# Performance work log

Measured on AMD Instinct MI355X. Metric: run time of the kernel, lower is better.

Reference implementation:

```python
import jax, jax.numpy as jnp
import numpy as np

B, N, D, H, M = 4, 4096, 1024, 16, 128
DH = D // H  # 64
SCALE = DH ** -0.5


def setup_inputs() -> dict:
    key = jax.random.key(0)
    ks = jax.random.split(key, 8)
    std = 0.02
    x = jax.random.normal(ks[0], (B, N, D), dtype=jnp.float32)
    W_qkv = jax.random.normal(ks[1], (D, 3 * D), dtype=jnp.float32) * std
    W_gate = jax.random.normal(ks[2], (D, H), dtype=jnp.float32) * std
    b_gate = jnp.zeros((H,), dtype=jnp.float32)
    agent_tokens = jax.random.normal(ks[3], (H, M, DH), dtype=jnp.float32) * std
    W_qa = jax.random.normal(ks[4], (H, H), dtype=jnp.float32) * std  # 1x1 conv over heads
    W_ak = jax.random.normal(ks[5], (H, H), dtype=jnp.float32) * std
    W_out = jax.random.normal(ks[6], (D, D), dtype=jnp.float32) * std
    mask = jnp.ones((B, N), dtype=bool)
    return {"x": x, "W_qkv": W_qkv, "W_gate": W_gate, "b_gate": b_gate,
            "agent_tokens": agent_tokens, "W_qa": W_qa, "W_ak": W_ak,
            "W_out": W_out, "mask": mask}


def reference(x, W_qkv, W_gate, b_gate, agent_tokens, W_qa, W_ak, W_out, mask):
    # qkv projection: b n (qkv h d) -> qkv b h n d
    qkv = (x @ W_qkv).reshape(B, N, 3, H, DH)
    qkv = jnp.transpose(qkv, (2, 0, 3, 1, 4))  # (3, B, H, N, DH)
    q, k, v = qkv[0], qkv[1], qkv[2]

    a = agent_tokens * SCALE  # (H, M, DH), broadcast over batch

    qa_sim = jnp.einsum('bhid,hjd->bhij', q, a)  # (B, H, N, M)
    ak_sim = jnp.einsum('hid,bhjd->bhij', a, k)  # (B, H, M, N)

    max_neg = -jnp.finfo(ak_sim.dtype).max
    ak_sim = jnp.where(mask[:, None, None, :], ak_sim, max_neg)

    qa_attn = jax.nn.softmax(qa_sim, axis=-1)
    ak_attn = jax.nn.softmax(ak_sim, axis=-1)

    # talking heads: 1x1 conv over head channel
    qa_attn = jnp.einsum('gh,bhij->bgij', W_qa, qa_attn)
    ak_attn = jnp.einsum('gh,bhij->bgij', W_ak, ak_attn)

    agent_gathered = jnp.einsum('bhij,bhjd->bhid', ak_attn, v)      # (B, H, M, DH)
    out = jnp.einsum('bhij,bhjd->bhid', qa_attn, agent_gathered)     # (B, H, N, DH)

    out = jnp.where(mask[:, None, :, None], out, 0.0)

    gates = jax.nn.sigmoid(x @ W_gate + b_gate)          # (B, N, H)
    out = out * jnp.transpose(gates, (0, 2, 1))[..., None]  # (B, H, N, 1)

    out = jnp.transpose(out, (0, 2, 1, 3)).reshape(B, N, D) @ W_out
    return out, agent_gathered
```

## Files before the change

kernel.cpp:

```cpp
#include <hip/hip_runtime.h>

#define B_   4
#define N_   4096
#define D_   1024
#define H_   16
#define DH_  64
#define M_   128
#define TD_  3072
#define SCALE_ 0.125f

typedef __attribute__((ext_vector_type(8))) short bf16x8;
typedef __attribute__((ext_vector_type(4))) float f32x4;

__device__ __forceinline__ ushort f2bf(float f) {
  union { float f; unsigned u; } v; v.f = f;
  unsigned r = (v.u + 0x7fff + ((v.u >> 16) & 1)) >> 16;
  return (ushort)r;
}

__device__ __forceinline__ float bf2f(ushort u) {
  union { unsigned u; float f; } v; v.u = ((unsigned)u) << 16;
  return v.f;
}

__global__ __launch_bounds__(256) void cvt_bf16_kernel(
    const float* __restrict__ in, ushort* __restrict__ out)
{
  long i = ((long)blockIdx.x * 256 + threadIdx.x) * 8;
  float4 a = *(const float4*)(in + i);
  float4 b = *(const float4*)(in + i + 4);
  bf16x8 o;
  o[0] = f2bf(a.x); o[1] = f2bf(a.y); o[2] = f2bf(a.z); o[3] = f2bf(a.w);
  o[4] = f2bf(b.x); o[5] = f2bf(b.y); o[6] = f2bf(b.z); o[7] = f2bf(b.w);
  *(bf16x8*)(out + i) = o;
}

__global__ __launch_bounds__(256) void cvtscale_kernel(
    const float* __restrict__ in, ushort* __restrict__ out,
    float* __restrict__ stats)
{
  if (blockIdx.x == 0)
    for (int i = threadIdx.x; i < 8192; i += 256) stats[i] = 0.f;
  long i = ((long)blockIdx.x * 256 + threadIdx.x) * 8;
  float4 a = *(const float4*)(in + i);
  float4 b = *(const float4*)(in + i + 4);
  bf16x8 o;
  o[0] = f2bf(a.x * SCALE_); o[1] = f2bf(a.y * SCALE_);
  o[2] = f2bf(a.z * SCALE_); o[3] = f2bf(a.w * SCALE_);
  o[4] = f2bf(b.x * SCALE_); o[5] = f2bf(b.y * SCALE_);
  o[6] = f2bf(b.z * SCALE_); o[7] = f2bf(b.w * SCALE_);
  *(bf16x8*)(out + i) = o;
}

__global__ __launch_bounds__(256) void wtrans_kernel(
    const float* __restrict__ W, int ld, int col_off, ushort* __restrict__ out)
{
  __shared__ float t[32][33];
  int tx = threadIdx.x & 31, ty = threadIdx.x >> 5;
  int n0 = blockIdx.x * 32, k0 = blockIdx.y * 32;
#pragma unroll
  for (int i = 0; i < 4; i++)
    t[ty + i * 8][tx] = W[(long)(k0 + ty + i * 8) * ld + col_off + n0 + tx];
  __syncthreads();
#pragma unroll
  for (int i = 0; i < 4; i++)
    out[(long)(n0 + ty + i * 8) * 1024 + k0 + tx] = f2bf(t[tx][ty + i * 8]);
}

__global__ __launch_bounds__(256) void wgtrans_kernel(
    const float* __restrict__ Wg, ushort* __restrict__ out)
{
  long idx = ((long)blockIdx.x * 256 + threadIdx.x) * 8;
  int n = (int)(idx >> 10), k0 = (int)(idx & 1023);
  bf16x8 o;
  if (n < 16) {
#pragma unroll
    for (int t = 0; t < 8; t++) o[t] = f2bf(Wg[(long)(k0 + t) * 16 + n]);
  } else {
#pragma unroll
    for (int t = 0; t < 8; t++) o[t] = 0;
  }
  *(bf16x8*)(out + idx) = o;
}

__global__ __launch_bounds__(256) void qkv_gemm_kernel(
    const ushort* __restrict__ A, const ushort* __restrict__ BT,
    ushort* __restrict__ QKV, float* __restrict__ gat,
    const float* __restrict__ bg)
{
  __shared__ ushort As[2][128 * 64];
  __shared__ ushort Bs[2][128 * 64];
  int tid = threadIdx.x;
  int lane = tid & 63, w = tid >> 6;
  int wr = w >> 1, wc = w & 1;
  int m0 = blockIdx.y * 128, n0g = blockIdx.x * 128;
  int sr = tid >> 3, sc = tid & 7;
  int gc = sc ^ (sr & 7);
  int quad = lane >> 4, row16 = lane & 15;

  const ushort* Ab = A + (long)m0 * 1024;
  const ushort* Bb = BT + (long)n0g * 1024;

  f32x4 acc[4][4] = {};

#define QKV_STAGE(buf, kk)                                                       \
  {                                                                              \
    _Pragma("unroll")                                                            \
    for (int i = 0; i < 4; i++) {                                                \
      int r = i * 32 + sr;                                                       \
      __builtin_amdgcn_global_load_lds(                                          \
          (const __attribute__((address_space(1))) void*)(Ab + (long)r * 1024 + (kk) + gc * 8), \
          (__attribute__((address_space(3))) void*)(As[buf] + (i * 32 + w * 8) * 64), \
          16, 0, 0);                                                             \
      __builtin_amdgcn_global_load_lds(                                          \
          (const __attribute__((address_space(1))) void*)(Bb + (long)r * 1024 + (kk) + gc * 8), \
          (__attribute__((address_space(3))) void*)(Bs[buf] + (i * 32 + w * 8) * 64), \
          16, 0, 0);                                                             \
    }                                                                            \
  }

  QKV_STAGE(0, 0)

  for (int k0 = 0; k0 < 1024; k0 += 64) {
    int cur = (k0 >> 6) & 1;
    __syncthreads();
    if (k0 + 64 < 1024) QKV_STAGE(cur ^ 1, k0 + 64)
#pragma unroll
    for (int ks = 0; ks < 2; ks++) {
      int ch = (ks * 4 + quad) ^ (lane & 7);
      bf16x8 af[4], bfr[4];
#pragma unroll
      for (int mi = 0; mi < 4; mi++)
        af[mi] = *(const bf16x8*)&As[cur][(wr * 64 + mi * 16 + row16) * 64 + ch * 8];
#pragma unroll
      for (int ni = 0; ni < 4; ni++)
        bfr[ni] = *(const bf16x8*)&Bs[cur][(wc * 64 + ni * 16 + row16) * 64 + ch * 8];
#pragma unroll
      for (int mi = 0; mi < 4; mi++)
#pragma unroll
        for (int ni = 0; ni < 4; ni++)
          acc[mi][ni] = __builtin_amdgcn_mfma_f32_16x16x32_bf16(
              af[mi], bfr[ni], acc[mi][ni], 0, 0, 0);
    }
  }
#undef QKV_STAGE

  if (n0g < 3072) {
    ushort* Cb = QKV + (long)(n0g >> 10) * (4096L * 1024);
    int n0 = n0g & 1023;
#pragma unroll
    for (int mi = 0; mi < 4; mi++)
#pragma unroll
      for (int ni = 0; ni < 4; ni++) {
        int m = m0 + wr * 64 + mi * 16 + quad * 4;
        int n = n0 + wc * 64 + ni * 16 + row16;
#pragma unroll
        for (int r = 0; r < 4; r++)
          Cb[(long)(m + r) * 1024 + n] = f2bf(acc[mi][ni][r]);
      }
  } else if (wc == 0) {
    float bgv = bg[row16];
#pragma unroll
    for (int mi = 0; mi < 4; mi++)
#pragma unroll
      for (int r = 0; r < 4; r++) {
        int m = m0 + wr * 64 + mi * 16 + quad * 4 + r;
        float a = acc[mi][0][r] + bgv;
        gat[(long)m * 16 + row16] = 1.f / (1.f + __expf(-a));
      }
  }
}

__global__ __launch_bounds__(256) void pair_gemm_kernel(
    const ushort* __restrict__ A0, const ushort* __restrict__ A1,
    const ushort* __restrict__ BT, float* __restrict__ C)
{
  __shared__ ushort As[2][128 * 64];
  __shared__ ushort Bs[2][128 * 64];
  int tid = threadIdx.x;
  int lane = tid & 63, w = tid >> 6;
  int wr = w >> 1, wc = w & 1;
  int m0 = blockIdx.y * 128, n0 = blockIdx.x * 128;
  int sr = tid >> 3, sc = tid & 7;
  int gc = sc ^ (sr & 7);
  int quad = lane >> 4, row16 = lane & 15;

  const ushort* Ab = (m0 < 4096) ? (A0 + (long)m0 * 1024)
                                 : (A1 + (long)(m0 - 4096) * 1024);
  const ushort* Bb = BT + (long)n0 * 1024;

  f32x4 acc[4][4] = {};

#define PAIR_STAGE(buf, kk)                                                      \
  {                                                                              \
    _Pragma("unroll")                                                            \
    for (int i = 0; i < 4; i++) {                                                \
      int r = i * 32 + sr;                                                       \
      __builtin_amdgcn_global_load_lds(                                          \
          (const __attribute__((address_space(1))) void*)(Ab + (long)r * 1024 + (kk) + gc * 8), \
          (__attribute__((address_space(3))) void*)(As[buf] + (i * 32 + w * 8) * 64), \
          16, 0, 0);                                                             \
      __builtin_amdgcn_global_load_lds(                                          \
          (const __attribute__((address_space(1))) void*)(Bb + (long)r * 1024 + (kk) + gc * 8), \
          (__attribute__((address_space(3))) void*)(Bs[buf] + (i * 32 + w * 8) * 64), \
          16, 0, 0);                                                             \
    }                                                                            \
  }

  PAIR_STAGE(0, 0)

  for (int k0 = 0; k0 < 1024; k0 += 64) {
    int cur = (k0 >> 6) & 1;
    __syncthreads();
    if (k0 + 64 < 1024) PAIR_STAGE(cur ^ 1, k0 + 64)
#pragma unroll
    for (int ks = 0; ks < 2; ks++) {
      int ch = (ks * 4 + quad) ^ (lane & 7);
      bf16x8 af[4], bfr[4];
#pragma unroll
      for (int mi = 0; mi < 4; mi++)
        af[mi] = *(const bf16x8*)&As[cur][(wr * 64 + mi * 16 + row16) * 64 + ch * 8];
#pragma unroll
      for (int ni = 0; ni < 4; ni++)
        bfr[ni] = *(const bf16x8*)&Bs[cur][(wc * 64 + ni * 16 + row16) * 64 + ch * 8];
#pragma unroll
      for (int mi = 0; mi < 4; mi++)
#pragma unroll
        for (int ni = 0; ni < 4; ni++)
          acc[mi][ni] = __builtin_amdgcn_mfma_f32_16x16x32_bf16(
              af[mi], bfr[ni], acc[mi][ni], 0, 0, 0);
    }
  }
#undef PAIR_STAGE

#pragma unroll
  for (int mi = 0; mi < 4; mi++)
#pragma unroll
    for (int ni = 0; ni < 4; ni++) {
      int m = m0 + wr * 64 + mi * 16 + quad * 4;
      int n = n0 + wc * 64 + ni * 16 + row16;
#pragma unroll
      for (int r = 0; r < 4; r++)
        C[(long)(m + r) * 1024 + n] = acc[mi][ni][r];
    }
}

__global__ __launch_bounds__(256) void dot64_mfma_kernel(
    const ushort* __restrict__ abf, const ushort* __restrict__ kbuf,
    ushort* __restrict__ C0, float* __restrict__ ssum)
{
  __shared__ ushort As[128 * 64];
  __shared__ ushort Bs[128 * 64];
  int tid = threadIdx.x;
  int lane = tid & 63, w = tid >> 6;
  int wr = w >> 1, wc = w & 1;
  int h = blockIdx.y;
  int n0 = blockIdx.x * 128;
  int sr = tid >> 3, sc = tid & 7;
  int gc = sc ^ (sr & 7);
  int quad = lane >> 4, row16 = lane & 15;
  const ushort* Aab = abf + (long)h * (M_ * DH_);
  const ushort* Bb  = kbuf + (long)n0 * D_ + h * DH_;

#pragma unroll
  for (int i = 0; i < 4; i++) {
    int r = i * 32 + sr;
    __builtin_amdgcn_global_load_lds(
        (const __attribute__((address_space(1))) void*)(Aab + (long)r * DH_ + gc * 8),
        (__attribute__((address_space(3))) void*)(As + (i * 32 + w * 8) * 64), 16, 0, 0);
    __builtin_amdgcn_global_load_lds(
        (const __attribute__((address_space(1))) void*)(Bb + (long)r * D_ + gc * 8),
        (__attribute__((address_space(3))) void*)(Bs + (i * 32 + w * 8) * 64), 16, 0, 0);
  }
  __syncthreads();

  f32x4 acc[4][4] = {};
#pragma unroll
  for (int ks = 0; ks < 2; ks++) {
    int ch = (ks * 4 + quad) ^ (lane & 7);
    bf16x8 af[4], bfr[4];
#pragma unroll
    for (int mi = 0; mi < 4; mi++)
      af[mi] = *(const bf16x8*)&As[(wr * 64 + mi * 16 + row16) * 64 + ch * 8];
#pragma unroll
    for (int ni = 0; ni < 4; ni++)
      bfr[ni] = *(const bf16x8*)&Bs[(wc * 64 + ni * 16 + row16) * 64 + ch * 8];
#pragma unroll
    for (int mi = 0; mi < 4; mi++)
#pragma unroll
      for (int ni = 0; ni < 4; ni++)
        acc[mi][ni] = __builtin_amdgcn_mfma_f32_16x16x32_bf16(
            af[mi], bfr[ni], acc[mi][ni], 0, 0, 0);
  }

  ushort* C = C0 + (long)h * (M_ * N_);
#pragma unroll
  for (int mi = 0; mi < 4; mi++)
#pragma unroll
    for (int ni = 0; ni < 4; ni++) {
      int j = wr * 64 + mi * 16 + quad * 4;
      int n = n0 + wc * 64 + ni * 16 + row16;
#pragma unroll
      for (int r = 0; r < 4; r++)
        C[(long)(j + r) * N_ + n] = f2bf(acc[mi][ni][r]);
    }

  float* Sb = ssum + h * M_;
#pragma unroll
  for (int mi = 0; mi < 4; mi++)
#pragma unroll
    for (int r = 0; r < 4; r++) {
      float p = 0.f;
#pragma unroll
      for (int ni = 0; ni < 4; ni++)
        p += __expf(bf2f(f2bf(acc[mi][ni][r])));
#pragma unroll
      for (int off = 8; off; off >>= 1) p += __shfl_xor(p, off);
      if (row16 == 0) {
        int j = wr * 64 + mi * 16 + quad * 4 + r;
        atomicAdd(Sb + j, p);
      }
    }
}

__global__ __launch_bounds__(256) void dot64sm_mfma_kernel(
    const ushort* __restrict__ qbuf, const ushort* __restrict__ abf,
    ushort* __restrict__ C0)
{
  __shared__ ushort As[128 * 64];
  __shared__ ushort Bs[128 * 64];
  int tid = threadIdx.x;
  int lane = tid & 63, w = tid >> 6;
  int h = blockIdx.y;
  int n0 = blockIdx.x * 128;
  int sr = tid >> 3, sc = tid & 7;
  int gc = sc ^ (sr & 7);
  int quad = lane >> 4, row16 = lane & 15;
  const ushort* Aab = qbuf + (long)n0 * D_ + h * DH_;
  const ushort* Bb  = abf + (long)h * (M_ * DH_);

#pragma unroll
  for (int i = 0; i < 4; i++) {
    int r = i * 32 + sr;
    __builtin_amdgcn_global_load_lds(
        (const __attribute__((address_space(1))) void*)(Aab + (long)r * D_ + gc * 8),
        (__attribute__((address_space(3))) void*)(As + (i * 32 + w * 8) * 64), 16, 0, 0);
    __builtin_amdgcn_global_load_lds(
        (const __attribute__((address_space(1))) void*)(Bb + (long)r * DH_ + gc * 8),
        (__attribute__((address_space(3))) void*)(Bs + (i * 32 + w * 8) * 64), 16, 0, 0);
  }
  __syncthreads();

  f32x4 acc[2][8] = {};
#pragma unroll
  for (int ks = 0; ks < 2; ks++) {
    int ch = (ks * 4 + quad) ^ (lane & 7);
    bf16x8 af[2], bfr[8];
#pragma unroll
    for (int mi = 0; mi < 2; mi++)
      af[mi] = *(const bf16x8*)&As[(w * 32 + mi * 16 + row16) * 64 + ch * 8];
#pragma unroll
    for (int ni = 0; ni < 8; ni++)
      bfr[ni] = *(const bf16x8*)&Bs[(ni * 16 + row16) * 64 + ch * 8];
#pragma unroll
    for (int mi = 0; mi < 2; mi++)
#pragma unroll
      for (int ni = 0; ni < 8; ni++)
        acc[mi][ni] = __builtin_amdgcn_mfma_f32_16x16x32_bf16(
            af[mi], bfr[ni], acc[mi][ni], 0, 0, 0);
  }

  ushort* C = C0 + (long)h * (N_ * M_);
#pragma unroll
  for (int mi = 0; mi < 2; mi++)
#pragma unroll
    for (int r = 0; r < 4; r++) {
      float mx = acc[mi][0][r];
#pragma unroll
      for (int ni = 1; ni < 8; ni++) mx = fmaxf(mx, acc[mi][ni][r]);
#pragma unroll
      for (int off = 8; off; off >>= 1) mx = fmaxf(mx, __shfl_xor(mx, off));
      float e[8], s = 0.f;
#pragma unroll
      for (int ni = 0; ni < 8; ni++) { e[ni] = __expf(acc[mi][ni][r] - mx); s += e[ni]; }
#pragma unroll
      for (int off = 8; off; off >>= 1) s += __shfl_xor(s, off);
      float inv = 1.f / s;
      int n = n0 + w * 32 + mi * 16 + quad * 4 + r;
      ushort* cp = C + (long)n * M_;
#pragma unroll
      for (int ni = 0; ni < 8; ni++)
        cp[ni * 16 + row16] = f2bf(e[ni] * inv);
    }
}

__global__ __launch_bounds__(256) void normmix_kernel(
    ushort* __restrict__ sim, const float* __restrict__ W,
    const float* __restrict__ ssum)
{
  __shared__ float Ws[256];
  __shared__ float is[16];
  int tid = threadIdx.x;
  Ws[tid] = W[tid];
  int j = blockIdx.x >> 2;
  if (tid < 16) is[tid] = 1.f / ssum[tid * 128 + j];
  __syncthreads();
  long n = (long)(blockIdx.x & 3) * 1024 + tid * 4;
  ushort* p = sim + (long)j * N_ + n;
  float e[16][4];
#pragma unroll
  for (int hh = 0; hh < 16; hh++) {
    ushort4 v = *(const ushort4*)(p + (long)hh * (M_ * N_));
    e[hh][0] = __expf(bf2f(v.x)) * is[hh];
    e[hh][1] = __expf(bf2f(v.y)) * is[hh];
    e[hh][2] = __expf(bf2f(v.z)) * is[hh];
    e[hh][3] = __expf(bf2f(v.w)) * is[hh];
  }
#pragma unroll
  for (int g = 0; g < 16; g++) {
    float a0 = 0.f, a1 = 0.f, a2 = 0.f, a3 = 0.f;
#pragma unroll
    for (int hh = 0; hh < 16; hh++) {
      float wv = Ws[g * 16 + hh];
      a0 += wv * e[hh][0]; a1 += wv * e[hh][1];
      a2 += wv * e[hh][2]; a3 += wv * e[hh][3];
    }
    ushort4 o;
    o.x = f2bf(a0); o.y = f2bf(a1); o.z = f2bf(a2); o.w = f2bf(a3);
    *(ushort4*)(p + (long)g * (M_ * N_)) = o;
  }
}

__global__ __launch_bounds__(256) void talking_heads_kernel(
    ushort* __restrict__ buf, const float* __restrict__ W)
{
  __shared__ float Ws[256];
  int tid = threadIdx.x;
  Ws[tid] = W[tid];
  __syncthreads();
  long r = ((long)blockIdx.x * 256 + tid) * 4;
  ushort* p = buf + r;
  float vin[16][4];
#pragma unroll
  for (int hh = 0; hh < 16; hh++) {
    ushort4 v = *(const ushort4*)(p + (long)hh * 524288);
    vin[hh][0] = bf2f(v.x); vin[hh][1] = bf2f(v.y);
    vin[hh][2] = bf2f(v.z); vin[hh][3] = bf2f(v.w);
  }
#pragma unroll
  for (int g = 0; g < 16; g++) {
    float a0 = 0.f, a1 = 0.f, a2 = 0.f, a3 = 0.f;
#pragma unroll
    for (int hh = 0; hh < 16; hh++) {
      float wv = Ws[g * 16 + hh];
      a0 += wv * vin[hh][0]; a1 += wv * vin[hh][1];
      a2 += wv * vin[hh][2]; a3 += wv * vin[hh][3];
    }
    ushort4 o;
    o.x = f2bf(a0); o.y = f2bf(a1); o.z = f2bf(a2); o.w = f2bf(a3);
    *(ushort4*)(p + (long)g * 524288) = o;
  }
}

__global__ __launch_bounds__(256) void ag_mfma_kernel(
    const ushort* __restrict__ ak2, const ushort* __restrict__ vbf,
    float* __restrict__ part)
{
  __shared__ ushort As[64 * 64];
  __shared__ ushort Bs[64 * 64];
  int tid = threadIdx.x;
  int lane = tid & 63, w = tid >> 6;
  int g = blockIdx.x, jh = blockIdx.y, kq = blockIdx.z;
  int quad = lane >> 4, row16 = lane & 15;
  const ushort* A = ak2 + ((long)g * M_ + jh * 64) * N_;
  const ushort* V = vbf + g * 64;
  int sr = tid >> 3, sc = tid & 7;
  int gc = sc ^ (sr & 7);
  f32x4 acc[4] = {};

  for (int kk = kq * 256; kk < kq * 256 + 256; kk += 64) {
    __syncthreads();
#pragma unroll
    for (int i = 0; i < 2; i++) {
      int r = i * 32 + sr;
      __builtin_amdgcn_global_load_lds(
          (const __attribute__((address_space(1))) void*)(A + (long)r * N_ + kk + gc * 8),
          (__attribute__((address_space(3))) void*)(As + (i * 32 + w * 8) * 64),
          16, 0, 0);
    }
    {
      int n = lane, c = n >> 3, p = n & 7;
      const ushort* pv = V + (long)(kk + n) * D_ + w * 16;
      bf16x8 v0 = *(const bf16x8*)(pv);
      bf16x8 v1 = *(const bf16x8*)(pv + 8);
#pragma unroll
      for (int jj = 0; jj < 8; jj++) {
        int d = w * 16 + jj, d2 = d + 8;
        Bs[d * 64 + ((c ^ (d & 7)) * 8 + p)]   = (ushort)v0[jj];
        Bs[d2 * 64 + ((c ^ (d2 & 7)) * 8 + p)] = (ushort)v1[jj];
      }
    }
    __syncthreads();
#pragma unroll
    for (int ks = 0; ks < 2; ks++) {
      int ch = (ks * 4 + quad) ^ (lane & 7);
      bf16x8 af = *(const bf16x8*)&As[(w * 16 + row16) * 64 + ch * 8];
      bf16x8 bfr[4];
#pragma unroll
      for (int ni = 0; ni < 4; ni++)
        bfr[ni] = *(const bf16x8*)&Bs[(ni * 16 + row16) * 64 + ch * 8];
#pragma unroll
      for (int ni = 0; ni < 4; ni++)
        acc[ni] = __builtin_amdgcn_mfma_f32_16x16x32_bf16(af, bfr[ni], acc[ni], 0, 0, 0);
    }
  }
  float* po = part + ((long)kq * 32 + g * 2 + jh) * 4096;
#pragma unroll
  for (int ni = 0; ni < 4; ni++) {
    int jl = w * 16 + quad * 4;
    int d = ni * 16 + row16;
#pragma unroll
    for (int r = 0; r < 4; r++)
      po[(jl + r) * 64 + d] = acc[ni][r];
  }
}

__global__ __launch_bounds__(256) void agred_kernel(
    const float* __restrict__ part, float* __restrict__ ag)
{
  long f = ((long)blockIdx.x * 256 + threadIdx.x) * 4;
  float4 s = make_float4(0.f, 0.f, 0.f, 0.f);
#pragma unroll
  for (int kq = 0; kq < 16; kq++) {
    float4 v = *(const float4*)(part + (long)kq * 131072 + f);
    s.x += v.x; s.y += v.y; s.z += v.z; s.w += v.w;
  }
  *(float4*)(ag + f) = s;
}

__global__ __launch_bounds__(256) void outpv_mfma_kernel(
    const ushort* __restrict__ qa2, const float* __restrict__ ag,
    const float* __restrict__ gat, ushort* __restrict__ ybf)
{
  __shared__ ushort As[2][128 * 64];
  __shared__ ushort Bs[2][64 * 64];
  int tid = threadIdx.x;
  int lane = tid & 63, w = tid >> 6;
  int wr = w >> 1, wc = w & 1;
  int h = blockIdx.y;
  int n0 = blockIdx.x * 128;
  int sr = tid >> 3, sc = tid & 7;
  int gc = sc ^ (sr & 7);
  int quad = lane >> 4, row16 = lane & 15;
  const ushort* P = qa2 + (long)h * (N_ * M_);
  const float* G = ag + (long)h * (M_ * DH_);

#pragma unroll
  for (int c = 0; c < 2; c++)
#pragma unroll
    for (int i = 0; i < 4; i++) {
      int r = i * 32 + sr;
      __builtin_amdgcn_global_load_lds(
          (const __attribute__((address_space(1))) void*)(P + (long)(n0 + r) * M_ + c * 64 + gc * 8),
          (__attribute__((address_space(3))) void*)(As[c] + (i * 32 + w * 8) * 64),
          16, 0, 0);
    }
  {
    int j = tid >> 1, d0 = (tid & 1) * 32;
    int chn = j >> 6, jl = j & 63, cc = jl >> 3, pp = jl & 7;
    const float* pg = G + (long)j * DH_ + d0;
#pragma unroll
    for (int i = 0; i < 32; i += 4) {
      float4 v = *(const float4*)(pg + i);
      float vv[4] = {v.x, v.y, v.z, v.w};
#pragma unroll
      for (int t = 0; t < 4; t++) {
        int d = d0 + i + t;
        Bs[chn][d * 64 + ((cc ^ (d & 7)) * 8 + pp)] = f2bf(vv[t]);
      }
    }
  }
  __syncthreads();

  f32x4 acc[4][2] = {};
#pragma unroll
  for (int ks = 0; ks < 4; ks++) {
    int chunk = ks >> 1;
    int ch = ((ks & 1) * 4 + quad) ^ (lane & 7);
    bf16x8 af[4], bfr[2];
#pragma unroll
    for (int mi = 0; mi < 4; mi++)
      af[mi] = *(const bf16x8*)&As[chunk][(wr * 64 + mi * 16 + row16) * 64 + ch * 8];
#pragma unroll
    for (int ni = 0; ni < 2; ni++)
      bfr[ni] = *(const bf16x8*)&Bs[chunk][(wc * 32 + ni * 16 + row16) * 64 + ch * 8];
#pragma unroll
    for (int mi = 0; mi < 4; mi++)
#pragma unroll
      for (int ni = 0; ni < 2; ni++)
        acc[mi][ni] = __builtin_amdgcn_mfma_f32_16x16x32_bf16(
            af[mi], bfr[ni], acc[mi][ni], 0, 0, 0);
  }

#pragma unroll
  for (int mi = 0; mi < 4; mi++)
#pragma unroll
    for (int r = 0; r < 4; r++) {
      int nn = n0 + wr * 64 + mi * 16 + quad * 4 + r;
      float gv = gat[(long)nn * 16 + h];
#pragma unroll
      for (int ni = 0; ni < 2; ni++) {
        int d = wc * 32 + ni * 16 + row16;
        ybf[(long)nn * 1024 + h * 64 + d] = f2bf(acc[mi][ni][r] * gv);
      }
    }
}

extern "C" void kernel_launch(void* const* d_in, const int* in_sizes, int n_in,
                              void* d_out, int out_size, void* d_ws, size_t ws_size,
                              hipStream_t stream)
{
  const float* x      = (const float*)d_in[0];
  const float* W_qkv  = (const float*)d_in[1];
  const float* W_gate = (const float*)d_in[2];
  const float* b_gate = (const float*)d_in[3];
  const float* agent  = (const float*)d_in[4];
  const float* W_qa   = (const float*)d_in[5];
  const float* W_ak   = (const float*)d_in[6];
  const float* W_out  = (const float*)d_in[7];

  if (ws_size < 68157440UL) return;

  float* out0 = (float*)d_out;
  float* ag   = out0 + (long)B_ * N_ * D_;

  ushort* qkvb  = (ushort*)d_ws;
  ushort* simh  = qkvb + 12582912;
  float*  gat   = (float*)(simh + 8388608);
  ushort* xbf   = (ushort*)(gat + 262144);
  ushort* wqkvT = xbf + 4194304;
  ushort* woutT = wqkvT + 3276800;
  ushort* abf   = woutT + 1048576;
  float*  stats = (float*)(abf + 131072);
  ushort* qpl = qkvb;
  ushort* kpl = qkvb + 4194304;
  ushort* vpl = qkvb + 8388608;
  float* part = (float*)kpl;

  wtrans_kernel<<<dim3(32, 32), 256, 0, stream>>>(W_qkv, TD_, 0,      wqkvT);
  wtrans_kernel<<<dim3(32, 32), 256, 0, stream>>>(W_qkv, TD_, D_,     wqkvT + 1048576);
  wtrans_kernel<<<dim3(32, 32), 256, 0, stream>>>(W_qkv, TD_, 2 * D_, wqkvT + 2097152);
  wgtrans_kernel<<<dim3(64), 256, 0, stream>>>(W_gate, wqkvT + 3145728);
  wtrans_kernel<<<dim3(32, 32), 256, 0, stream>>>(W_out, D_,  0,      woutT);
  cvtscale_kernel<<<dim3(64), 256, 0, stream>>>(agent, abf, stats);

  for (int b = 0; b < B_; b++) {
    const float* xb = x + (long)b * N_ * D_;
    float* agb = ag + (long)b * H_ * M_ * DH_;
    float* ssum = stats + (long)b * 2048;
    float* gatb = gat + (long)b * N_ * H_;
    ushort* xdst = (b & 1) ? simh : xbf;
    ushort* ydst = (b & 1) ? qpl : xbf;

    cvt_bf16_kernel<<<dim3(2048), 256, 0, stream>>>(xb, xdst);
    qkv_gemm_kernel<<<dim3(25, 32), 256, 0, stream>>>(xdst, wqkvT, qkvb, gatb, b_gate);
    dot64_mfma_kernel<<<dim3(32, 16), 256, 0, stream>>>(abf, kpl, simh, ssum);
    normmix_kernel<<<dim3(512), 256, 0, stream>>>(simh, W_ak, ssum);
    ag_mfma_kernel<<<dim3(16, 2, 16), 256, 0, stream>>>(simh, vpl, part);
    agred_kernel<<<dim3(128), 256, 0, stream>>>(part, agb);
    dot64sm_mfma_kernel<<<dim3(32, 16), 256, 0, stream>>>(qpl, abf, simh);
    talking_heads_kernel<<<dim3((M_ * N_) / 1024), 256, 0, stream>>>(simh, W_qa);
    outpv_mfma_kernel<<<dim3(32, 16), 256, 0, stream>>>(
        simh, agb, gatb, ydst);
    if (b & 1)
      pair_gemm_kernel<<<dim3(8, 64), 256, 0, stream>>>(
          xbf, qpl, woutT, out0 + (long)(b - 1) * N_ * D_);
  }
}
```

Before: 644.1 us.

## Fuse prep kernels, merge agent reduction into dot kernel, swizzle GEMM block order

Merges weight transposes, gate weight packing, agent scaling and the first batch's x conversion into one prep launch, and folds the agent-gathered partial reduction into the dot64sm kernel as extra blocks. Also remaps GEMM block indices with a stride-8 swizzle to change L2 locality of tiles. The goal is fewer kernel launches and less idle tail time, with better cache reuse in the projections. This adds branching heterogeneous blocks within single kernels.

```diff
diff --git a/kernel.cpp b/kernel.cpp
--- a/kernel.cpp
+++ b/kernel.cpp
@@ -35,52 +35,66 @@
   *(bf16x8*)(out + i) = o;
 }
 
-__global__ __launch_bounds__(256) void cvtscale_kernel(
-    const float* __restrict__ in, ushort* __restrict__ out,
-    float* __restrict__ stats)
-{
-  if (blockIdx.x == 0)
-    for (int i = threadIdx.x; i < 8192; i += 256) stats[i] = 0.f;
-  long i = ((long)blockIdx.x * 256 + threadIdx.x) * 8;
-  float4 a = *(const float4*)(in + i);
-  float4 b = *(const float4*)(in + i + 4);
-  bf16x8 o;
-  o[0] = f2bf(a.x * SCALE_); o[1] = f2bf(a.y * SCALE_);
-  o[2] = f2bf(a.z * SCALE_); o[3] = f2bf(a.w * SCALE_);
-  o[4] = f2bf(b.x * SCALE_); o[5] = f2bf(b.y * SCALE_);
-  o[6] = f2bf(b.z * SCALE_); o[7] = f2bf(b.w * SCALE_);
-  *(bf16x8*)(out + i) = o;
-}
-
-__global__ __launch_bounds__(256) void wtrans_kernel(
-    const float* __restrict__ W, int ld, int col_off, ushort* __restrict__ out)
-{
-  __shared__ float t[32][33];
-  int tx = threadIdx.x & 31, ty = threadIdx.x >> 5;
-  int n0 = blockIdx.x * 32, k0 = blockIdx.y * 32;
-#pragma unroll
-  for (int i = 0; i < 4; i++)
-    t[ty + i * 8][tx] = W[(long)(k0 + ty + i * 8) * ld + col_off + n0 + tx];
-  __syncthreads();
-#pragma unroll
-  for (int i = 0; i < 4; i++)
-    out[(long)(n0 + ty + i * 8) * 1024 + k0 + tx] = f2bf(t[tx][ty + i * 8]);
-}
-
-__global__ __launch_bounds__(256) void wgtrans_kernel(
-    const float* __restrict__ Wg, ushort* __restrict__ out)
-{
-  long idx = ((long)blockIdx.x * 256 + threadIdx.x) * 8;
-  int n = (int)(idx >> 10), k0 = (int)(idx & 1023);
-  bf16x8 o;
-  if (n < 16) {
-#pragma unroll
-    for (int t = 0; t < 8; t++) o[t] = f2bf(Wg[(long)(k0 + t) * 16 + n]);
+__global__ __launch_bounds__(256) void prep_kernel(
+    const float* __restrict__ W_qkv, const float* __restrict__ W_out,
+    const float* __restrict__ Wg, const float* __restrict__ agent,
+    const float* __restrict__ x0,
+    ushort* __restrict__ wqkvT, ushort* __restrict__ woutT,
+    ushort* __restrict__ abf, float* __restrict__ stats,
+    ushort* __restrict__ xbf)
+{
+  int bid = blockIdx.x;
+  int tid = threadIdx.x;
+  if (bid < 4096) {
+    __shared__ float t[32][33];
+    int sec = bid >> 10, local = bid & 1023;
+    int bx = local & 31, by = local >> 5;
+    const float* W; int ld, col_off; ushort* out;
+    if (sec < 3) { W = W_qkv; ld = TD_; col_off = sec * D_; out = wqkvT + sec * 1048576; }
+    else         { W = W_out; ld = D_;  col_off = 0;        out = woutT; }
+    int tx = tid & 31, ty = tid >> 5;
+    int n0 = bx * 32, k0 = by * 32;
+#pragma unroll
+    for (int i = 0; i < 4; i++)
+      t[ty + i * 8][tx] = W[(long)(k0 + ty + i * 8) * ld + col_off + n0 + tx];
+    __syncthreads();
+#pragma unroll
+    for (int i = 0; i < 4; i++)
+      out[(long)(n0 + ty + i * 8) * 1024 + k0 + tx] = f2bf(t[tx][ty + i * 8]);
+  } else if (bid < 4160) {
+    long idx = ((long)(bid - 4096) * 256 + tid) * 8;
+    int n = (int)(idx >> 10), k0 = (int)(idx & 1023);
+    bf16x8 o;
+    if (n < 16) {
+#pragma unroll
+      for (int t2 = 0; t2 < 8; t2++) o[t2] = f2bf(Wg[(long)(k0 + t2) * 16 + n]);
+    } else {
+#pragma unroll
+      for (int t2 = 0; t2 < 8; t2++) o[t2] = 0;
+    }
+    *(bf16x8*)(wqkvT + 3145728 + idx) = o;
+  } else if (bid < 4224) {
+    int lb = bid - 4160;
+    if (lb == 0)
+      for (int i = tid; i < 8192; i += 256) stats[i] = 0.f;
+    long i = ((long)lb * 256 + tid) * 8;
+    float4 a = *(const float4*)(agent + i);
+    float4 b = *(const float4*)(agent + i + 4);
+    bf16x8 o;
+    o[0] = f2bf(a.x * SCALE_); o[1] = f2bf(a.y * SCALE_);
+    o[2] = f2bf(a.z * SCALE_); o[3] = f2bf(a.w * SCALE_);
+    o[4] = f2bf(b.x * SCALE_); o[5] = f2bf(b.y * SCALE_);
+    o[6] = f2bf(b.z * SCALE_); o[7] = f2bf(b.w * SCALE_);
+    *(bf16x8*)(abf + i) = o;
   } else {
-#pragma unroll
-    for (int t = 0; t < 8; t++) o[t] = 0;
-  }
-  *(bf16x8*)(out + idx) = o;
+    long i = ((long)(bid - 4224) * 256 + tid) * 8;
+    float4 a = *(const float4*)(x0 + i);
+    float4 b = *(const float4*)(x0 + i + 4);
+    bf16x8 o;
+    o[0] = f2bf(a.x); o[1] = f2bf(a.y); o[2] = f2bf(a.z); o[3] = f2bf(a.w);
+    o[4] = f2bf(b.x); o[5] = f2bf(b.y); o[6] = f2bf(b.z); o[7] = f2bf(b.w);
+    *(bf16x8*)(xbf + i) = o;
+  }
 }
 
 __global__ __launch_bounds__(256) void qkv_gemm_kernel(
@@ -93,7 +107,9 @@
   int tid = threadIdx.x;
   int lane = tid & 63, w = tid >> 6;
   int wr = w >> 1, wc = w & 1;
-  int m0 = blockIdx.y * 128, n0g = blockIdx.x * 128;
+  int bid = blockIdx.y * 25 + blockIdx.x;
+  int swz = (bid & 7) * 100 + (bid >> 3);
+  int m0 = (swz / 25) * 128, n0g = (swz % 25) * 128;
   int sr = tid >> 3, sc = tid & 7;
   int gc = sc ^ (sr & 7);
   int quad = lane >> 4, row16 = lane & 15;
@@ -180,7 +196,9 @@
   int tid = threadIdx.x;
   int lane = tid & 63, w = tid >> 6;
   int wr = w >> 1, wc = w & 1;
-  int m0 = blockIdx.y * 128, n0 = blockIdx.x * 128;
+  int bid = blockIdx.y * 8 + blockIdx.x;
+  int swz = (bid & 7) * 64 + (bid >> 3);
+  int m0 = (swz >> 3) * 128, n0 = (swz & 7) * 128;
   int sr = tid >> 3, sc = tid & 7;
   int gc = sc ^ (sr & 7);
   int quad = lane >> 4, row16 = lane & 15;
@@ -323,16 +341,28 @@
     }
 }
 
-__global__ __launch_bounds__(256) void dot64sm_mfma_kernel(
+__global__ __launch_bounds__(256) void dot64sm_agred_kernel(
     const ushort* __restrict__ qbuf, const ushort* __restrict__ abf,
-    ushort* __restrict__ C0)
-{
+    ushort* __restrict__ C0,
+    const float* __restrict__ part, float* __restrict__ ag)
+{
+  int tid = threadIdx.x;
+  if (blockIdx.x >= 512) {
+    long f = ((long)(blockIdx.x - 512) * 256 + tid) * 4;
+    float4 s = make_float4(0.f, 0.f, 0.f, 0.f);
+#pragma unroll
+    for (int kq = 0; kq < 16; kq++) {
+      float4 v = *(const float4*)(part + (long)kq * 131072 + f);
+      s.x += v.x; s.y += v.y; s.z += v.z; s.w += v.w;
+    }
+    *(float4*)(ag + f) = s;
+    return;
+  }
   __shared__ ushort As[128 * 64];
   __shared__ ushort Bs[128 * 64];
-  int tid = threadIdx.x;
   int lane = tid & 63, w = tid >> 6;
-  int h = blockIdx.y;
-  int n0 = blockIdx.x * 128;
+  int h = blockIdx.x >> 5;
+  int n0 = (blockIdx.x & 31) * 128;
   int sr = tid >> 3, sc = tid & 7;
   int gc = sc ^ (sr & 7);
   int quad = lane >> 4, row16 = lane & 15;
@@ -523,19 +553,6 @@
     for (int r = 0; r < 4; r++)
       po[(jl + r) * 64 + d] = acc[ni][r];
   }
-}
-
-__global__ __launch_bounds__(256) void agred_kernel(
-    const float* __restrict__ part, float* __restrict__ ag)
-{
-  long f = ((long)blockIdx.x * 256 + threadIdx.x) * 4;
-  float4 s = make_float4(0.f, 0.f, 0.f, 0.f);
-#pragma unroll
-  for (int kq = 0; kq < 16; kq++) {
-    float4 v = *(const float4*)(part + (long)kq * 131072 + f);
-    s.x += v.x; s.y += v.y; s.z += v.z; s.w += v.w;
-  }
-  *(float4*)(ag + f) = s;
 }
 
 __global__ __launch_bounds__(256) void outpv_mfma_kernel(
@@ -647,12 +664,8 @@
   ushort* vpl = qkvb + 8388608;
   float* part = (float*)kpl;
 
-  wtrans_kernel<<<dim3(32, 32), 256, 0, stream>>>(W_qkv, TD_, 0,      wqkvT);
-  wtrans_kernel<<<dim3(32, 32), 256, 0, stream>>>(W_qkv, TD_, D_,     wqkvT + 1048576);
-  wtrans_kernel<<<dim3(32, 32), 256, 0, stream>>>(W_qkv, TD_, 2 * D_, wqkvT + 2097152);
-  wgtrans_kernel<<<dim3(64), 256, 0, stream>>>(W_gate, wqkvT + 3145728);
-  wtrans_kernel<<<dim3(32, 32), 256, 0, stream>>>(W_out, D_,  0,      woutT);
-  cvtscale_kernel<<<dim3(64), 256, 0, stream>>>(agent, abf, stats);
+  prep_kernel<<<dim3(6272), 256, 0, stream>>>(
+      W_qkv, W_out, W_gate, agent, x, wqkvT, woutT, abf, stats, xbf);
 
   for (int b = 0; b < B_; b++) {
     const float* xb = x + (long)b * N_ * D_;
@@ -662,13 +675,13 @@
     ushort* xdst = (b & 1) ? simh : xbf;
     ushort* ydst = (b & 1) ? qpl : xbf;
 
-    cvt_bf16_kernel<<<dim3(2048), 256, 0, stream>>>(xb, xdst);
+    if (b > 0)
+      cvt_bf16_kernel<<<dim3(2048), 256, 0, stream>>>(xb, xdst);
     qkv_gemm_kernel<<<dim3(25, 32), 256, 0, stream>>>(xdst, wqkvT, qkvb, gatb, b_gate);
     dot64_mfma_kernel<<<dim3(32, 16), 256, 0, stream>>>(abf, kpl, simh, ssum);
     normmix_kernel<<<dim3(512), 256, 0, stream>>>(simh, W_ak, ssum);
     ag_mfma_kernel<<<dim3(16, 2, 16), 256, 0, stream>>>(simh, vpl, part);
-    agred_kernel<<<dim3(128), 256, 0, stream>>>(part, agb);
-    dot64sm_mfma_kernel<<<dim3(32, 16), 256, 0, stream>>>(qpl, abf, simh);
+    dot64sm_agred_kernel<<<dim3(640), 256, 0, stream>>>(qpl, abf, simh, part, agb);
     talking_heads_kernel<<<dim3((M_ * N_) / 1024), 256, 0, stream>>>(simh, W_qa);
     outpv_mfma_kernel<<<dim3(32, 16), 256, 0, stream>>>(
         simh, agb, gatb, ydst);
```

New measurement: 614.6 us. 4.6% less time.
